# Kernel optimization log

Measured on AMD Instinct MI355X. Metric: run time of the kernel, lower is better.

Reference implementation:

```python
import jax, jax.numpy as jnp
import numpy as np

B, N, C = 4, 2048, 1152
H = 16
DH = C // H  # 72
EPS = 1e-6
THETA = 10000.0


def _rms_norm(x, w):
    # per-head RMSNorm in fp32, matching LlamaRMSNorm
    xf = x.astype(jnp.float32)
    var = jnp.mean(xf * xf, axis=-1, keepdims=True)
    return (w * (xf * jax.lax.rsqrt(var + EPS)).astype(x.dtype))


def _rope_cos_sin(n, dh, dtype):
    half = dh // 2
    inv_freq = 1.0 / (THETA ** (jnp.arange(0, half, dtype=jnp.float32) / half))
    ang = jnp.arange(n, dtype=jnp.float32)[:, None] * inv_freq[None, :]  # [N, half]
    return jnp.cos(ang).astype(dtype), jnp.sin(ang).astype(dtype)


def _apply_rope(x, cos, sin):
    # x: [B,H,N,DH]; rotate-half style
    half = x.shape[-1] // 2
    x1, x2 = x[..., :half], x[..., half:]
    return jnp.concatenate([x1 * cos - x2 * sin, x2 * cos + x1 * sin], axis=-1)


def setup_inputs() -> dict:
    key = jax.random.key(0)
    ks = jax.random.split(key, 3)
    x = jax.random.normal(ks[0], (B, N, C), dtype=jnp.float32)
    w_qkv = jax.random.normal(ks[1], (3 * C, C), dtype=jnp.float32) * (C ** -0.5)
    w_proj = jax.random.normal(ks[2], (C, C), dtype=jnp.float32) * (C ** -0.5)
    b_proj = jnp.zeros((C,), dtype=jnp.float32)
    q_norm_w = jnp.ones((DH,), dtype=jnp.float32)
    k_norm_w = jnp.ones((DH,), dtype=jnp.float32)
    return {"x": x, "w_qkv": w_qkv, "w_proj": w_proj, "b_proj": b_proj,
            "q_norm_w": q_norm_w, "k_norm_w": k_norm_w}


def reference(x, w_qkv, w_proj, b_proj, q_norm_w, k_norm_w):
    b, n, c = x.shape
    # QKV projection (no bias)
    qkv = jnp.einsum('bnc,dc->bnd', x, w_qkv)  # [B,N,3C]
    qkv = qkv.reshape(b, n, 3, H, DH).transpose(2, 0, 3, 1, 4)  # [3,B,H,N,DH]
    q, k, v = qkv[0], qkv[1], qkv[2]
    # RoPE on q, k
    cos, sin = _rope_cos_sin(n, DH, x.dtype)  # [N, DH/2]
    q = _apply_rope(q, cos, sin)
    k = _apply_rope(k, cos, sin)
    # per-head QK RMSNorm
    q = _rms_norm(q, q_norm_w)
    k = _rms_norm(k, k_norm_w)
    # scaled dot-product attention
    scale = DH ** -0.5
    attn = jax.nn.softmax(jnp.einsum('bhqd,bhkd->bhqk', q, k) * scale, axis=-1)
    out = jnp.einsum('bhqk,bhkd->bhqd', attn, v)  # [B,H,N,DH]
    out = out.transpose(0, 2, 1, 3).reshape(b, n, c)
    return jnp.einsum('bnc,dc->bnd', out, w_proj) + b_proj
```

## Files before the change

kernel.cpp:

```cpp
#include <hip/hip_runtime.h>
#include <stdint.h>

#define BATCH 4
#define NSEQ  2048
#define CDIM  1152
#define HB    16
#define DHD   72
#define D3    3456
#define NT    8192

typedef __attribute__((ext_vector_type(8))) short short8;
typedef __attribute__((ext_vector_type(8))) unsigned short u16x8;
typedef __attribute__((ext_vector_type(4))) unsigned short u16x4;
typedef __attribute__((ext_vector_type(2))) unsigned int u32x2;
typedef __attribute__((ext_vector_type(4))) float f32x4;

__device__ __forceinline__ float bf2f(unsigned short u) {
  return __uint_as_float(((unsigned)u) << 16);
}
__device__ __forceinline__ unsigned short f2bf(float f) {
  unsigned u = __float_as_uint(f);
  u += 0x7FFF + ((u >> 16) & 1);
  return (unsigned short)(u >> 16);
}
__device__ __forceinline__ unsigned pkbf(float lo, float hi) {
  unsigned r;
  asm("v_cvt_pk_bf16_f32 %0, %1, %2" : "=v"(r) : "v"(lo), "v"(hi));
  return r;
}

__device__ __forceinline__ void gload_lds16(const unsigned short* g, unsigned short* l) {
  __builtin_amdgcn_global_load_lds(
      (const __attribute__((address_space(1))) void*)g,
      (__attribute__((address_space(3))) void*)l, 16, 0, 0);
}

#define XN    ((size_t)NT * CDIM)
#define WQN   ((size_t)D3 * CDIM)
#define WPN   ((size_t)CDIM * CDIM)
#define CVT_CHUNKS ((XN + WQN + WPN) / 4)

__global__ __launch_bounds__(256) void cvt_bf16(
    const float* __restrict__ x, const float* __restrict__ wq,
    const float* __restrict__ wp, unsigned short* __restrict__ xb,
    unsigned short* __restrict__ wqb, unsigned short* __restrict__ wpb) {
  size_t c = (size_t)blockIdx.x * 256 + threadIdx.x;
  if (c >= CVT_CHUNKS) return;
  const float* src;
  unsigned short* dst;
  size_t e = c * 4;
  if (e < XN) { src = x + e; dst = xb + e; }
  else if (e < XN + WQN) { src = wq + (e - XN); dst = wqb + (e - XN); }
  else { src = wp + (e - XN - WQN); dst = wpb + (e - XN - WQN); }
  f32x4 v = *(const f32x4*)src;
  u16x4 r;
#pragma unroll
  for (int i = 0; i < 4; i++) r[i] = f2bf(v[i]);
  *(u16x4*)dst = r;
}

template <int SCATTER>
__global__ __launch_bounds__(256) void gemm_bt(
    const unsigned short* __restrict__ A, const unsigned short* __restrict__ Bt,
    const float* __restrict__ bias, void* __restrict__ Cout,
    unsigned short* __restrict__ Vt, int M, int Dn, int K) {
  __shared__ __attribute__((aligned(16))) unsigned short sA[128 * 64];
  __shared__ __attribute__((aligned(16))) unsigned short sB[128 * 64];

  const int tid  = threadIdx.x;
  const int lane = tid & 63;
  const int w    = tid >> 6;
  const int wm   = w >> 1, wn = w & 1;
  const int quad = lane >> 4, l16 = lane & 15;
  const int s7l  = l16 & 7;

  const int gx  = gridDim.x;
  const int lb  = blockIdx.y * gx + blockIdx.x;
  const int xcd = lb & 7;
  const int pos = lb >> 3;
  const int m0 = ((xcd << 3) + (pos & 7)) * 128;
  const int n0 = (pos >> 3) * 128;

  const int r8 = lane >> 3;
  const int cu = (lane & 7) ^ r8;
  const unsigned short* gA = A  + (size_t)(m0 + w * 32 + r8) * K + cu * 8;
  const unsigned short* gB = Bt + (size_t)(n0 + w * 32 + r8) * K + cu * 8;

  const f32x4 zero = {0.f, 0.f, 0.f, 0.f};
  f32x4 acc[4][4];
#pragma unroll
  for (int i = 0; i < 4; i++)
#pragma unroll
    for (int j = 0; j < 4; j++) acc[i][j] = zero;

  for (int kt = 0; kt < K; kt += 64) {
#pragma unroll
    for (int i = 0; i < 4; i++) {
      gload_lds16(gA + (size_t)i * 8 * K + kt, sA + (w * 4 + i) * 512);
      gload_lds16(gB + (size_t)i * 8 * K + kt, sB + (w * 4 + i) * 512);
    }
    __syncthreads();

#pragma unroll
    for (int kk = 0; kk < 2; kk++) {
      short8 a[4], b[4];
#pragma unroll
      for (int i = 0; i < 4; i++) {
        a[i] = *(const short8*)(sA + (wm * 64 + i * 16 + l16) * 64 +
                                (((kk * 4 + quad) ^ s7l) << 3));
        b[i] = *(const short8*)(sB + (wn * 64 + i * 16 + l16) * 64 +
                                (((kk * 4 + quad) ^ s7l) << 3));
      }
#pragma unroll
      for (int i = 0; i < 4; i++)
#pragma unroll
        for (int j = 0; j < 4; j++)
          acc[i][j] = __builtin_amdgcn_mfma_f32_16x16x32_bf16(a[i], b[j], acc[i][j], 0, 0, 0);
    }
    __syncthreads();
  }

#pragma unroll
  for (int i = 0; i < 4; i++) {
    int row = m0 + wm * 64 + i * 16 + quad * 4;
#pragma unroll
    for (int j = 0; j < 4; j++) {
      int col = n0 + wn * 64 + j * 16 + l16;
      if (SCATTER) {
        int s  = col / CDIM;
        int rm = col - s * CDIM;
        int h  = rm / DHD;
        int dh = rm - h * DHD;
        int b_ = row >> 11;
        int n  = row & 2047;
        if (s == 2) {
#pragma unroll
          for (int r = 0; r < 4; r++)
            Vt[((size_t)(b_ * HB + h) * DHD + dh) * NSEQ + n + r] = f2bf(acc[i][j][r]);
        } else {
          unsigned short* Cb = (unsigned short*)Cout;
#pragma unroll
          for (int r = 0; r < 4; r++)
            Cb[(((size_t)(s * BATCH + b_) * HB + h) * NSEQ + (n + r)) * DHD + dh] =
                f2bf(acc[i][j][r]);
        }
      } else {
        float bb = bias ? bias[col] : 0.f;
        float* Cf = (float*)Cout;
#pragma unroll
        for (int r = 0; r < 4; r++)
          Cf[(size_t)(row + r) * Dn + col] = acc[i][j][r] + bb;
      }
    }
  }
}

__global__ __launch_bounds__(256) void rope_rms(
    unsigned short* __restrict__ qkvb,
    const float* __restrict__ qw, const float* __restrict__ kw) {
  const int blk = blockIdx.x;
  const int b = blk >> 11;
  const int n = blk & 2047;
  const int tid = threadIdx.x;

  __shared__ float sv[2][CDIM];
  __shared__ float srsq[2][HB];

  const float nf = (float)n;
  const float l2t_over_half = 13.287712379549449f / 36.0f;
  const float scale2 = 0.17002329230297715f;

  for (int g = tid; g < 288; g += 256) {
    int sel = (g >= 144) ? 1 : 0;
    int gg  = g - sel * 144;
    int h   = gg / 9;
    int u   = gg - h * 9;
    const unsigned short* src =
        qkvb + (((size_t)(sel * BATCH + b) * HB + h) * NSEQ + n) * DHD + u * 8;
    u16x8 v = *(const u16x8*)src;
    float* dst = &sv[sel][h * DHD + u * 8];
#pragma unroll
    for (int r = 0; r < 8; r++) dst[r] = bf2f(v[r]);
  }
  __syncthreads();

  for (int p = tid; p < 1152; p += 256) {
    int sel = (p >= 576) ? 1 : 0;
    int pp  = p - sel * 576;
    int h   = pp / 36;
    int i   = pp - h * 36;
    float* row = &sv[sel][h * DHD];
    float x1 = row[i], x2 = row[i + 36];
    float ang = nf * exp2f(-l2t_over_half * (float)i);
    float sn, cs;
    __sincosf(ang, &sn, &cs);
    row[i]      = x1 * cs - x2 * sn;
    row[i + 36] = x2 * cs + x1 * sn;
  }
  __syncthreads();

  if (tid < 128) {
    int sel = tid >> 6;
    int h = (tid & 63) >> 2, p = tid & 3;
    float s = 0.f;
#pragma unroll
    for (int d = 0; d < 18; d++) {
      float v = sv[sel][h * DHD + p * 18 + d];
      s += v * v;
    }
    s += __shfl_xor(s, 1);
    s += __shfl_xor(s, 2);
    if (p == 0)
      srsq[sel][h] = rsqrtf(s * (1.0f / 72.0f) + 1e-6f) * (sel ? 1.0f : scale2);
  }
  __syncthreads();

  for (int g = tid; g < 288; g += 256) {
    int sel = (g >= 144) ? 1 : 0;
    int gg  = g - sel * 144;
    int h   = gg / 9;
    int u   = gg - h * 9;
    float rs = srsq[sel][h];
    const float* wn = (sel ? kw : qw) + u * 8;
    const float* s = &sv[sel][h * DHD + u * 8];
    u16x8 o;
#pragma unroll
    for (int r = 0; r < 8; r++) o[r] = f2bf(s[r] * rs * wn[r]);
    unsigned short* dst =
        qkvb + (((size_t)(sel * BATCH + b) * HB + h) * NSEQ + n) * DHD + u * 8;
    *(u16x8*)dst = o;
  }
}

__global__ __launch_bounds__(256, 4) void flash_attn(
    const unsigned short* __restrict__ qkvb, const unsigned short* __restrict__ Vt,
    unsigned short* __restrict__ AO) {
  __shared__ __attribute__((aligned(16))) unsigned short sK[64 * 72];
  __shared__ __attribute__((aligned(16))) unsigned short sVt[80 * 64];
  __shared__ __attribute__((aligned(16))) unsigned short sP[128 * 64];

  const int tid  = threadIdx.x;
  const int w    = tid >> 6;
  const int lane = tid & 63;
  const int quad = lane >> 4, l16 = lane & 15;
  const int s7   = l16 & 7;
  const int q0 = blockIdx.x * 128;
  const int h = blockIdx.y, b = blockIdx.z;

  const unsigned short* Qb = qkvb + ((size_t)(0 * BATCH + b) * HB + h) * NSEQ * DHD;
  const unsigned short* Kb = qkvb + ((size_t)(1 * BATCH + b) * HB + h) * NSEQ * DHD;
  const unsigned short* Vb = Vt + (size_t)(b * HB + h) * DHD * NSEQ;

  const short8 zs = {0, 0, 0, 0, 0, 0, 0, 0};
  const f32x4 zero = {0.f, 0.f, 0.f, 0.f};

  const int vswz = ((lane & 7) ^ (lane >> 3)) * 8;
  const unsigned short* pKn[3];
  const unsigned short* pVn[3];
#pragma unroll
  for (int j = 0; j < 3; j++) {
    int i = w + 4 * j;
    int ii = (i < 9) ? i : 0;
    pKn[j] = Kb + ii * 512 + lane * 8;
    pVn[j] = Vb + (size_t)(ii * 8 + (lane >> 3)) * NSEQ + vswz;
  }

#pragma unroll
  for (int j = 0; j < 3; j++) {
    int i = w + 4 * j;
    if (i < 9) {
      gload_lds16(pKn[j], sK + i * 512);
      gload_lds16(pVn[j], sVt + i * 512);
      pKn[j] += 64 * 72;
      pVn[j] += 64;
    }
  }

  for (int e = tid; e < 512; e += 256)
    sVt[72 * 64 + e] = (e < 64) ? (unsigned short)0x3F80 : (unsigned short)0;

  short8 aq[2][3];
#pragma unroll
  for (int qt = 0; qt < 2; qt++) {
    const unsigned short* qrow = Qb + (size_t)(q0 + w * 32 + qt * 16 + l16) * DHD;
    aq[qt][0] = *(const short8*)(qrow + quad * 8);
    aq[qt][1] = *(const short8*)(qrow + 32 + quad * 8);
    aq[qt][2] = (quad == 0) ? *(const short8*)(qrow + 64) : zs;
  }

  f32x4 o[2][5];
#pragma unroll
  for (int qt = 0; qt < 2; qt++)
#pragma unroll
    for (int nb = 0; nb < 5; nb++) o[qt][nb] = zero;

  auto sphase_pack = [&]() {
    f32x4 st[2][4];
    __builtin_amdgcn_s_setprio(1);
#pragma unroll
    for (int nk = 0; nk < 4; nk++) {
      const unsigned short* kr = sK + (nk * 16 + l16) * 72;
      short8 kf0 = *(const short8*)(kr + quad * 8);
      short8 kf1 = *(const short8*)(kr + 32 + quad * 8);
      short8 kf2 = *(const short8*)(kr + 64);
      f32x4 s0 = zero, s1 = zero;
      s0 = __builtin_amdgcn_mfma_f32_16x16x32_bf16(kf0, aq[0][0], s0, 0, 0, 0);
      s1 = __builtin_amdgcn_mfma_f32_16x16x32_bf16(kf0, aq[1][0], s1, 0, 0, 0);
      s0 = __builtin_amdgcn_mfma_f32_16x16x32_bf16(kf1, aq[0][1], s0, 0, 0, 0);
      s1 = __builtin_amdgcn_mfma_f32_16x16x32_bf16(kf1, aq[1][1], s1, 0, 0, 0);
      s0 = __builtin_amdgcn_mfma_f32_16x16x32_bf16(kf2, aq[0][2], s0, 0, 0, 0);
      s1 = __builtin_amdgcn_mfma_f32_16x16x32_bf16(kf2, aq[1][2], s1, 0, 0, 0);
      st[0][nk] = s0;
      st[1][nk] = s1;
    }
    __builtin_amdgcn_s_setprio(0);
#pragma unroll
    for (int qt = 0; qt < 2; qt++) {
      unsigned short* prow = sP + (qt * 64 + w * 16 + l16) * 64 + (quad & 1) * 4;
#pragma unroll
      for (int nk = 0; nk < 4; nk++) {
        int uoff = ((nk * 2 + (quad >> 1)) ^ s7) << 3;
        u32x2 pr;
        pr[0] = pkbf(exp2f(st[qt][nk][0]), exp2f(st[qt][nk][1]));
        pr[1] = pkbf(exp2f(st[qt][nk][2]), exp2f(st[qt][nk][3]));
        *(u32x2*)(prow + uoff) = pr;
      }
    }
  };

  auto pv_phase = [&]() {
    __builtin_amdgcn_s_setprio(1);
#pragma unroll
    for (int kb = 0; kb < 2; kb++) {
      const unsigned short* pp =
          sP + (w * 16 + l16) * 64 + (((kb * 4 + quad) ^ s7) << 3);
      short8 pf0 = *(const short8*)pp;
      short8 pf1 = *(const short8*)(pp + 64 * 64);
#pragma unroll
      for (int nb = 0; nb < 5; nb++) {
        short8 vf = *(const short8*)(sVt + (nb * 16 + l16) * 64 +
                                     (((kb * 4 + quad) ^ s7) << 3));
        o[0][nb] = __builtin_amdgcn_mfma_f32_16x16x32_bf16(pf0, vf, o[0][nb], 0, 0, 0);
        o[1][nb] = __builtin_amdgcn_mfma_f32_16x16x32_bf16(pf1, vf, o[1][nb], 0, 0, 0);
      }
    }
    __builtin_amdgcn_s_setprio(0);
  };

  __syncthreads();

  for (int t = 0; t < 32; t++) {
    sphase_pack();

    __syncthreads();

    if (t < 31) {
#pragma unroll
      for (int j = 0; j < 3; j++) {
        int i = w + 4 * j;
        if (i < 9) { gload_lds16(pKn[j], sK + i * 512); pKn[j] += 64 * 72; }
      }
    }

    pv_phase();

    __syncthreads();

    if (t < 31) {
#pragma unroll
      for (int j = 0; j < 3; j++) {
        int i = w + 4 * j;
        if (i < 9) { gload_lds16(pVn[j], sVt + i * 512); pVn[j] += 64; }
      }
    }
  }

#pragma unroll
  for (int qt = 0; qt < 2; qt++) {
    float inv[4];
#pragma unroll
    for (int r = 0; r < 4; r++)
      inv[r] = 1.0f / __shfl(o[qt][4][r], (quad << 4) + 8, 64);
    const int qrow = q0 + w * 32 + qt * 16 + quad * 4;
#pragma unroll
    for (int nb = 0; nb < 5; nb++) {
      int dh = nb * 16 + l16;
      if (dh < DHD) {
#pragma unroll
        for (int r = 0; r < 4; r++)
          AO[((size_t)b * NSEQ + qrow + r) * CDIM + h * DHD + dh] =
              f2bf(o[qt][nb][r] * inv[r]);
      }
    }
  }
}

extern "C" void kernel_launch(void* const* d_in, const int* in_sizes, int n_in,
                              void* d_out, int out_size, void* d_ws, size_t ws_size,
                              hipStream_t stream) {
  const float* x      = (const float*)d_in[0];
  const float* w_qkv  = (const float*)d_in[1];
  const float* w_proj = (const float*)d_in[2];
  const float* b_proj = (const float*)d_in[3];
  const float* qnw    = (const float*)d_in[4];
  const float* knw    = (const float*)d_in[5];
  float* out = (float*)d_out;

  char* ws = (char*)d_ws;
  unsigned short* xb    = (unsigned short*)(ws);
  unsigned short* wqkvb = (unsigned short*)(ws + 18874368);
  unsigned short* wprojb= (unsigned short*)(ws + 26836992);
  unsigned short* qkvb  = (unsigned short*)(ws + 29491200);
  unsigned short* Vt    = (unsigned short*)(ws + 67239936);
  unsigned short* AO    = xb;

  cvt_bf16<<<dim3((CVT_CHUNKS + 255) / 256), 256, 0, stream>>>(
      x, w_qkv, w_proj, xb, wqkvb, wprojb);
  gemm_bt<1><<<dim3(D3 / 128, NT / 128), 256, 0, stream>>>(
      xb, wqkvb, nullptr, qkvb, Vt, NT, D3, CDIM);
  rope_rms<<<dim3(NT), 256, 0, stream>>>(qkvb, qnw, knw);
  flash_attn<<<dim3(NSEQ / 128, HB, BATCH), 256, 0, stream>>>(qkvb, Vt, AO);
  gemm_bt<0><<<dim3(CDIM / 128, NT / 128), 256, 0, stream>>>(
      AO, wprojb, b_proj, out, nullptr, NT, CDIM, CDIM);
}
```

Baseline: 367.6 us.

## Add 256x256 double-buffered QKV GEMM kernel with overlapped LDS prefetch

Replaces the 128x128 templated GEMM for the QKV projection with a dedicated 512-thread kernel using 256x256 tiles. The next k-slice is loaded into a second LDS buffer while MFMAs run on the current one, and s_setprio raises priority around the MFMA bursts. The aim is more data reuse per tile and hidden global-load latency. In exchange it uses about 128KB of LDS per block, has a partial last column tile (3456 is not a multiple of 256) that reads past the weight rows and is masked only on store, and increases register pressure. The output projection keeps the old kernel, now untemplated.

```diff
diff --git a/kernel.cpp b/kernel.cpp
--- a/kernel.cpp
+++ b/kernel.cpp
@@ -59,11 +59,116 @@
   *(u16x4*)dst = r;
 }
 
-template <int SCATTER>
+__global__ __launch_bounds__(512, 2) void gemm256_qkv(
+    const unsigned short* __restrict__ A, const unsigned short* __restrict__ Bt,
+    unsigned short* __restrict__ qkvb, unsigned short* __restrict__ Vt) {
+  __shared__ __attribute__((aligned(16))) unsigned short sA[2 * 256 * 64];
+  __shared__ __attribute__((aligned(16))) unsigned short sB[2 * 256 * 64];
+
+  const int K = CDIM;
+  const int tid  = threadIdx.x;
+  const int lane = tid & 63;
+  const int w    = tid >> 6;
+  const int wm   = w >> 2, wn = w & 3;
+  const int quad = lane >> 4, l16 = lane & 15;
+  const int s7l  = l16 & 7;
+
+  const int lb  = blockIdx.y * gridDim.x + blockIdx.x;
+  const int xcd = lb & 7;
+  const int pos = lb >> 3;
+  const int m0 = (xcd * 4 + (pos & 3)) * 256;
+  const int n0 = (pos >> 2) * 256;
+
+  const int r8 = lane >> 3;
+  const int cu = (lane & 7) ^ r8;
+  const unsigned short* gA = A  + (size_t)(m0 + w * 8 + r8) * K + cu * 8;
+  const unsigned short* gB = Bt + (size_t)(n0 + w * 8 + r8) * K + cu * 8;
+
+  const f32x4 zero = {0.f, 0.f, 0.f, 0.f};
+  f32x4 acc[8][4];
+#pragma unroll
+  for (int i = 0; i < 8; i++)
+#pragma unroll
+    for (int j = 0; j < 4; j++) acc[i][j] = zero;
+
+#pragma unroll
+  for (int g = 0; g < 4; g++) {
+    gload_lds16(gA + (size_t)g * 64 * K, sA + g * 4096 + w * 512);
+    gload_lds16(gB + (size_t)g * 64 * K, sB + g * 4096 + w * 512);
+  }
+  __syncthreads();
+
+  for (int t = 0; t < 18; t++) {
+    const unsigned short* A_ = sA + (t & 1) * 16384;
+    const unsigned short* B_ = sB + (t & 1) * 16384;
+    unsigned short* An = sA + ((t + 1) & 1) * 16384;
+    unsigned short* Bn = sB + ((t + 1) & 1) * 16384;
+    const int ktn = (t + 1) * 64;
+
+#pragma unroll
+    for (int kk = 0; kk < 2; kk++) {
+      short8 a[8], b[4];
+#pragma unroll
+      for (int i = 0; i < 8; i++)
+        a[i] = *(const short8*)(A_ + (wm * 128 + i * 16 + l16) * 64 +
+                                (((kk * 4 + quad) ^ s7l) << 3));
+#pragma unroll
+      for (int j = 0; j < 4; j++)
+        b[j] = *(const short8*)(B_ + (wn * 64 + j * 16 + l16) * 64 +
+                                (((kk * 4 + quad) ^ s7l) << 3));
+
+      if (t < 17) {
+#pragma unroll
+        for (int g = 0; g < 4; g++) {
+          if (kk == 0)
+            gload_lds16(gA + (size_t)g * 64 * K + ktn, An + g * 4096 + w * 512);
+          else
+            gload_lds16(gB + (size_t)g * 64 * K + ktn, Bn + g * 4096 + w * 512);
+        }
+      }
+
+      __builtin_amdgcn_s_setprio(1);
+#pragma unroll
+      for (int i = 0; i < 8; i++)
+#pragma unroll
+        for (int j = 0; j < 4; j++)
+          acc[i][j] = __builtin_amdgcn_mfma_f32_16x16x32_bf16(a[i], b[j], acc[i][j], 0, 0, 0);
+      __builtin_amdgcn_s_setprio(0);
+    }
+    __syncthreads();
+  }
+
+#pragma unroll
+  for (int i = 0; i < 8; i++) {
+    int row = m0 + wm * 128 + i * 16 + quad * 4;
+    int b_ = row >> 11;
+    int n  = row & 2047;
+#pragma unroll
+    for (int j = 0; j < 4; j++) {
+      int col = n0 + wn * 64 + j * 16 + l16;
+      if (col < D3) {
+        int s  = col / CDIM;
+        int rm = col - s * CDIM;
+        int h  = rm / DHD;
+        int dh = rm - h * DHD;
+        if (s == 2) {
+#pragma unroll
+          for (int r = 0; r < 4; r++)
+            Vt[((size_t)(b_ * HB + h) * DHD + dh) * NSEQ + n + r] = f2bf(acc[i][j][r]);
+        } else {
+#pragma unroll
+          for (int r = 0; r < 4; r++)
+            qkvb[(((size_t)(s * BATCH + b_) * HB + h) * NSEQ + (n + r)) * DHD + dh] =
+                f2bf(acc[i][j][r]);
+        }
+      }
+    }
+  }
+}
+
 __global__ __launch_bounds__(256) void gemm_bt(
     const unsigned short* __restrict__ A, const unsigned short* __restrict__ Bt,
-    const float* __restrict__ bias, void* __restrict__ Cout,
-    unsigned short* __restrict__ Vt, int M, int Dn, int K) {
+    const float* __restrict__ bias, float* __restrict__ Cout, int M, int Dn, int K) {
   __shared__ __attribute__((aligned(16))) unsigned short sA[128 * 64];
   __shared__ __attribute__((aligned(16))) unsigned short sB[128 * 64];
 
@@ -126,31 +231,10 @@
 #pragma unroll
     for (int j = 0; j < 4; j++) {
       int col = n0 + wn * 64 + j * 16 + l16;
-      if (SCATTER) {
-        int s  = col / CDIM;
-        int rm = col - s * CDIM;
-        int h  = rm / DHD;
-        int dh = rm - h * DHD;
-        int b_ = row >> 11;
-        int n  = row & 2047;
-        if (s == 2) {
-#pragma unroll
-          for (int r = 0; r < 4; r++)
-            Vt[((size_t)(b_ * HB + h) * DHD + dh) * NSEQ + n + r] = f2bf(acc[i][j][r]);
-        } else {
-          unsigned short* Cb = (unsigned short*)Cout;
-#pragma unroll
-          for (int r = 0; r < 4; r++)
-            Cb[(((size_t)(s * BATCH + b_) * HB + h) * NSEQ + (n + r)) * DHD + dh] =
-                f2bf(acc[i][j][r]);
-        }
-      } else {
-        float bb = bias ? bias[col] : 0.f;
-        float* Cf = (float*)Cout;
-#pragma unroll
-        for (int r = 0; r < 4; r++)
-          Cf[(size_t)(row + r) * Dn + col] = acc[i][j][r] + bb;
-      }
+      float bb = bias ? bias[col] : 0.f;
+#pragma unroll
+      for (int r = 0; r < 4; r++)
+        Cout[(size_t)(row + r) * Dn + col] = acc[i][j][r] + bb;
     }
   }
 }
@@ -416,10 +500,9 @@
 
   cvt_bf16<<<dim3((CVT_CHUNKS + 255) / 256), 256, 0, stream>>>(
       x, w_qkv, w_proj, xb, wqkvb, wprojb);
-  gemm_bt<1><<<dim3(D3 / 128, NT / 128), 256, 0, stream>>>(
-      xb, wqkvb, nullptr, qkvb, Vt, NT, D3, CDIM);
+  gemm256_qkv<<<dim3(14, 32), 512, 0, stream>>>(xb, wqkvb, qkvb, Vt);
   rope_rms<<<dim3(NT), 256, 0, stream>>>(qkvb, qnw, knw);
   flash_attn<<<dim3(NSEQ / 128, HB, BATCH), 256, 0, stream>>>(qkvb, Vt, AO);
-  gemm_bt<0><<<dim3(CDIM / 128, NT / 128), 256, 0, stream>>>(
-      AO, wprojb, b_proj, out, nullptr, NT, CDIM, CDIM);
-}
+  gemm_bt<<<dim3(CDIM / 128, NT / 128), 256, 0, stream>>>(
+      AO, wprojb, b_proj, out, NT, CDIM, CDIM);
+}
```

After: 354.3 us. 1.04x faster.
